# Kernel tuning notes

Hardware: AMD Instinct MI355X
Metric: run time of the kernel (lower is better)

Reference implementation:

```python
import jax, jax.numpy as jnp
import numpy as np

HEADS = 4
LN_EPS = 1e-5

def layernorm(x, w, b):
    m = x.mean(-1, keepdims=True)
    v = ((x - m) ** 2).mean(-1, keepdims=True)
    return (x - m) * jax.lax.rsqrt(v + LN_EPS) * w + b

def conv3d(x, w, b, pad, dil=1, groups=1):
    out = jax.lax.conv_general_dilated(
        x, w, (1, 1, 1), [(pad, pad)] * 3,
        rhs_dilation=(dil, dil, dil),
        dimension_numbers=('NCDHW', 'OIDHW', 'NCDHW'),
        feature_group_count=groups)
    return out + b[None, :, None, None, None]

def trilinear_gather(x_flat, pz, py, px, D, H, W):
    # x_flat: [B,C,S]; pz/py/px: [B,S] fractional sample coords, zero padding outside
    z0f, y0f, x0f = jnp.floor(pz), jnp.floor(py), jnp.floor(px)
    wz, wy, wx = pz - z0f, py - y0f, px - x0f
    z0, y0, x0 = z0f.astype(jnp.int32), y0f.astype(jnp.int32), x0f.astype(jnp.int32)
    acc = jnp.zeros_like(x_flat)
    for dz in (0, 1):
        for dy in (0, 1):
            for dx in (0, 1):
                iz, iy, ix = z0 + dz, y0 + dy, x0 + dx
                cw = (wz if dz else 1.0 - wz) * (wy if dy else 1.0 - wy) * (wx if dx else 1.0 - wx)
                valid = (iz >= 0) & (iz < D) & (iy >= 0) & (iy < H) & (ix >= 0) & (ix < W)
                idx = (jnp.clip(iz, 0, D - 1) * H + jnp.clip(iy, 0, H - 1)) * W + jnp.clip(ix, 0, W - 1)
                vals = jnp.take_along_axis(x_flat, idx[:, None, :], axis=2)
                acc = acc + vals * (cw * valid)[:, None, :]
    return acc

def deform_conv3d(x, off_w, off_b, w, b):
    # DeformConvPack: offsets from a regular 3x3x3 conv, then offset trilinear sampling + conv
    B, C, D, H, W = x.shape
    K = 27
    offsets = conv3d(x, off_w, off_b, 1).reshape(B, K, 3, D * H * W)
    gz, gy, gx = jnp.indices((D, H, W))
    bz = gz.reshape(-1).astype(x.dtype)[None]
    by = gy.reshape(-1).astype(x.dtype)[None]
    bx = gx.reshape(-1).astype(x.dtype)[None]
    x_flat = x.reshape(B, C, -1)
    O = w.shape[0]
    wk = w.reshape(O, C, K)
    out = jnp.zeros((B, O, D * H * W), x.dtype)
    for k in range(K):  # fixed 27 kernel taps
        kz, ky, kx = k // 9, (k // 3) % 3, k % 3
        pz = bz + (kz - 1) + offsets[:, k, 0]
        py = by + (ky - 1) + offsets[:, k, 1]
        px = bx + (kx - 1) + offsets[:, k, 2]
        samp = trilinear_gather(x_flat, pz, py, px, D, H, W)  # [B,C,S]
        out = out + jnp.einsum('bcs,oc->bos', samp, wk[:, :, k])
    out = out + b[None, :, None]
    return out.reshape(B, O, D, H, W)

def forward(x, temperature, qkv_w, norm_w, norm_b, proj1_w, proj1_b, conv0_w, conv0_b,
            convsp_w, convsp_b, off_w, off_b, dcn_w, dcn_b, conv1_w, conv1_b,
            proj2_w, proj2_b, norm2_w, norm2_b, out_w, out_b, H, W, D):
    B, N, C = x.shape
    hd = C // HEADS
    qkv = (x @ qkv_w.T).reshape(B, N, 3, HEADS, hd).transpose(2, 0, 3, 1, 4)  # [3,B,h,N,hd]
    q = qkv[0].transpose(0, 1, 3, 2)  # [B,h,hd,N]
    k = qkv[1].transpose(0, 1, 3, 2)
    v = qkv[2].transpose(0, 1, 3, 2)
    q = q / jnp.maximum(jnp.sqrt((q * q).sum(-1, keepdims=True)), 1e-12)
    k = k / jnp.maximum(jnp.sqrt((k * k).sum(-1, keepdims=True)), 1e-12)
    attn = jnp.einsum('bhcn,bhdn->bhcd', q, k) * temperature[None]
    attn = jax.nn.softmax(attn, axis=-1)
    x_ca = jnp.einsum('bhcd,bhdn->bhcn', attn, v).transpose(0, 3, 1, 2).reshape(B, N, C)
    x_ca = layernorm(x_ca, norm_w, norm_b)
    x5 = x_ca.transpose(0, 2, 1).reshape(B, C, H, W, D)
    shortcut = x5
    y = jnp.einsum('bcxyz,oc->boxyz', x5, proj1_w) + proj1_b[None, :, None, None, None]
    y = jax.nn.gelu(y, approximate=False)
    u = y
    a = conv3d(y, conv0_w, conv0_b, 2, 1, C)      # depthwise k=5 pad=2
    a = conv3d(a, convsp_w, convsp_b, 9, 3, C)    # depthwise k=7 pad=9 dil=3
    a = deform_conv3d(a, off_w, off_b, dcn_w, dcn_b)
    a = jnp.einsum('bcxyz,oc->boxyz', a, conv1_w) + conv1_b[None, :, None, None, None]
    y = u * a
    y = jnp.einsum('bcxyz,oc->boxyz', y, proj2_w) + proj2_b[None, :, None, None, None]
    y = y + shortcut
    x_sa = y.reshape(B, C, N).transpose(0, 2, 1)           # lka returns [B,N,C]
    x_sa = x_sa.reshape(B, C, N).transpose(0, 2, 1)        # faithful torch reshape-after-permute
    x_sa = layernorm(x_sa, norm2_w, norm2_b)
    return x_sa @ out_w.T + out_b

def setup_inputs():
    key = jax.random.key(0)
    ks = jax.random.split(key, 12)
    B, C, H, W, D = 2, 64, 32, 32, 32
    N = H * W * D
    s = 0.02
    return dict(
        x=jax.random.normal(ks[0], (B, N, C), jnp.float32),
        temperature=jnp.ones((HEADS, 1, 1), jnp.float32),
        qkv_w=jax.random.normal(ks[1], (3 * C, C), jnp.float32) * s,
        norm_w=jnp.ones((C,), jnp.float32), norm_b=jnp.zeros((C,), jnp.float32),
        proj1_w=jax.random.normal(ks[2], (C, C), jnp.float32) * s,
        proj1_b=jnp.zeros((C,), jnp.float32),
        conv0_w=jax.random.normal(ks[3], (C, 1, 5, 5, 5), jnp.float32) * s,
        conv0_b=jnp.zeros((C,), jnp.float32),
        convsp_w=jax.random.normal(ks[4], (C, 1, 7, 7, 7), jnp.float32) * s,
        convsp_b=jnp.zeros((C,), jnp.float32),
        off_w=jax.random.normal(ks[5], (81, C, 3, 3, 3), jnp.float32) * 0.01,
        off_b=jnp.zeros((81,), jnp.float32),
        dcn_w=jax.random.normal(ks[6], (C, C, 3, 3, 3), jnp.float32) * s,
        dcn_b=jnp.zeros((C,), jnp.float32),
        conv1_w=jax.random.normal(ks[7], (C, C), jnp.float32) * s,
        conv1_b=jnp.zeros((C,), jnp.float32),
        proj2_w=jax.random.normal(ks[8], (C, C), jnp.float32) * s,
        proj2_b=jnp.zeros((C,), jnp.float32),
        norm2_w=jnp.ones((C,), jnp.float32), norm2_b=jnp.zeros((C,), jnp.float32),
        out_w=jax.random.normal(ks[9], (C, C), jnp.float32) * s,
        out_b=jnp.zeros((C,), jnp.float32),
        B_in=B, C_in=C, H=H, W=W, D=D,
    )

def reference(x, temperature, qkv_w, norm_w, norm_b, proj1_w, proj1_b, conv0_w, conv0_b,
              convsp_w, convsp_b, off_w, off_b, dcn_w, dcn_b, conv1_w, conv1_b,
              proj2_w, proj2_b, norm2_w, norm2_b, out_w, out_b, B_in, C_in, H, W, D):
    return forward(x, temperature, qkv_w, norm_w, norm_b, proj1_w, proj1_b, conv0_w, conv0_b,
                   convsp_w, convsp_b, off_w, off_b, dcn_w, dcn_b, conv1_w, conv1_b,
                   proj2_w, proj2_b, norm2_w, norm2_b, out_w, out_b, H, W, D)
```

## Files before the change

kernel.cpp:

```cpp
#include <hip/hip_runtime.h>
#include <hip/hip_bf16.h>

#define S 32768
#define BUFN (2*64*32768)

typedef __bf16 v8bf __attribute__((ext_vector_type(8)));
typedef float v4f __attribute__((ext_vector_type(4)));
typedef int v4i __attribute__((ext_vector_type(4)));

__device__ __forceinline__ ushort f2b(float f) {
  union { float f; unsigned u; } v; v.f = f;
  unsigned r = (v.u + 0x7fffu + ((v.u >> 16) & 1u)) >> 16;
  return (ushort)r;
}
__device__ __forceinline__ float b2f(ushort h) {
  union { unsigned u; float f; } v; v.u = ((unsigned)h) << 16;
  return v.f;
}
__device__ __forceinline__ float u2f(unsigned u) {
  union { unsigned u; float f; } v; v.u = u;
  return v.f;
}

__global__ void k_wt(const float* __restrict__ offw, const float* __restrict__ dcnw,
                     ushort* __restrict__ wt_off16, ushort* __restrict__ wt_dcn16) {
  int i = blockIdx.x*256 + threadIdx.x;
  if (i < 27*96*64) {
    int c = i & 63, o = (i >> 6) % 96, t = i / 6144;
    wt_off16[i] = (o < 81) ? f2b(offw[o*1728 + c*27 + t]) : (ushort)0;
  }
  if (i < 27*64*64) {
    int c = i & 63, o = (i >> 6) & 63, k = i >> 12;
    wt_dcn16[i] = f2b(dcnw[(o*64 + c)*27 + k]);
  }
}

__global__ __launch_bounds__(256) void k_qkv(const float* __restrict__ x,
    const float* __restrict__ qkv_w, float* __restrict__ q,
    float* __restrict__ k, float* __restrict__ v) {
  __shared__ float wsm[96*64];
  int half = blockIdx.x >> 8;
  int gid  = ((blockIdx.x & 255) << 8) + threadIdx.x;
  int rbase = half * 96;
  for (int i = threadIdx.x; i < 96*64; i += 256) wsm[i] = qkv_w[rbase*64 + i];
  __syncthreads();
  int b = gid >> 15, n = gid & (S-1);
  const float* xr = x + (size_t)gid * 64;
  float xv[64];
#pragma unroll
  for (int i = 0; i < 16; i++) {
    float4 t = ((const float4*)xr)[i];
    xv[4*i]=t.x; xv[4*i+1]=t.y; xv[4*i+2]=t.z; xv[4*i+3]=t.w;
  }
  for (int r = 0; r < 96; r++) {
    const float4* wr4 = (const float4*)&wsm[r*64];
    float acc = 0.f;
#pragma unroll
    for (int c4 = 0; c4 < 16; c4++) {
      float4 wv4 = wr4[c4];
      acc += xv[4*c4]*wv4.x + xv[4*c4+1]*wv4.y + xv[4*c4+2]*wv4.z + xv[4*c4+3]*wv4.w;
    }
    int row = rbase + r;
    float* dst = (row < 64) ? q : (row < 128 ? k : v);
    int ch = row & 63;
    dst[((size_t)(b*64 + ch))*S + n] = acc;
  }
}

__global__ __launch_bounds__(256) void k_rownorm(const float* __restrict__ q,
    const float* __restrict__ k, float* __restrict__ inv) {
  int row = blockIdx.x;
  const float* p = (row < 128) ? (q + (size_t)row*S) : (k + (size_t)(row-128)*S);
  const float4* p4 = (const float4*)p;
  float ss = 0.f;
  for (int i = threadIdx.x; i < S/4; i += 256) {
    float4 t = p4[i];
    ss += t.x*t.x + t.y*t.y + t.z*t.z + t.w*t.w;
  }
  __shared__ float red[256];
  red[threadIdx.x] = ss; __syncthreads();
  for (int st = 128; st > 0; st >>= 1) {
    if (threadIdx.x < st) red[threadIdx.x] += red[threadIdx.x+st];
    __syncthreads();
  }
  if (threadIdx.x == 0) inv[row] = 1.0f / fmaxf(sqrtf(red[0]), 1e-12f);
}

__global__ __launch_bounds__(256) void k_gram(const float* __restrict__ q,
    const float* __restrict__ k, float* __restrict__ gram) {
  __shared__ float qt[16][65], kt[16][65];
  int bi = blockIdx.x;
  int b = bi >> 7, h = (bi >> 5) & 3, chunk = bi & 31;
  int c = threadIdx.x >> 4, d = threadIdx.x & 15;
  const float* qb = q + ((size_t)(b*64 + h*16))*S;
  const float* kb = k + ((size_t)(b*64 + h*16))*S;
  int lr = threadIdx.x >> 4, lc = (threadIdx.x & 15) * 4;
  float acc = 0.f;
  for (int n0 = chunk*1024; n0 < chunk*1024 + 1024; n0 += 64) {
    float4 tq = *(const float4*)(qb + (size_t)lr*S + n0 + lc);
    float4 tk = *(const float4*)(kb + (size_t)lr*S + n0 + lc);
    __syncthreads();
    qt[lr][lc]=tq.x; qt[lr][lc+1]=tq.y; qt[lr][lc+2]=tq.z; qt[lr][lc+3]=tq.w;
    kt[lr][lc]=tk.x; kt[lr][lc+1]=tk.y; kt[lr][lc+2]=tk.z; kt[lr][lc+3]=tk.w;
    __syncthreads();
#pragma unroll
    for (int nn = 0; nn < 64; nn++) acc += qt[c][nn]*kt[d][nn];
  }
  atomicAdd(&gram[((b*4+h)*16+c)*16 + d], acc);
}

__global__ __launch_bounds__(256) void k_xca_ln(const float* __restrict__ v,
    const float* __restrict__ gram, const float* __restrict__ inv,
    const float* __restrict__ temp,
    const float* __restrict__ nw, const float* __restrict__ nb,
    float* __restrict__ x5) {
  __shared__ float at[1024];
  __shared__ float wsh[64], bsh[64];
  int gid = blockIdx.x*256 + threadIdx.x;
  int b = gid >> 15, n = gid & (S-1);
  int tid = threadIdx.x;
  if (tid < 64) {
    int h = tid >> 4, c = tid & 15;
    float iq = inv[b*64 + h*16 + c];
    float tp = temp[h];
    float l[16], m = -1e30f;
#pragma unroll
    for (int d = 0; d < 16; d++) {
      float vv = gram[((b*4+h)*16+c)*16 + d] * iq * inv[128 + b*64 + h*16 + d] * tp;
      l[d] = vv; m = fmaxf(m, vv);
    }
    float s = 0.f;
#pragma unroll
    for (int d = 0; d < 16; d++) { l[d] = expf(l[d]-m); s += l[d]; }
    float is = 1.0f / s;
#pragma unroll
    for (int d = 0; d < 16; d++) at[(h*16+c)*16 + d] = l[d]*is;
  } else if (tid < 128) {
    wsh[tid-64] = nw[tid-64]; bsh[tid-64] = nb[tid-64];
  }
  __syncthreads();
  const float* vb = v + (size_t)b*64*S + n;
  float vv[64];
#pragma unroll
  for (int ch = 0; ch < 64; ch++) vv[ch] = vb[(size_t)ch*S];
  float xc[64];
#pragma unroll
  for (int h = 0; h < 4; h++)
#pragma unroll
    for (int cc = 0; cc < 16; cc++) {
      float a = 0.f;
#pragma unroll
      for (int d = 0; d < 16; d++) a += at[(h*16+cc)*16 + d] * vv[h*16+d];
      xc[h*16+cc] = a;
    }
  float mean = 0.f;
#pragma unroll
  for (int ch = 0; ch < 64; ch++) mean += xc[ch];
  mean *= (1.0f/64.0f);
  float var = 0.f;
#pragma unroll
  for (int ch = 0; ch < 64; ch++) { float d = xc[ch]-mean; var += d*d; }
  var *= (1.0f/64.0f);
  float rs = rsqrtf(var + 1e-5f);
  float* xb = x5 + (size_t)b*64*S + n;
#pragma unroll
  for (int ch = 0; ch < 64; ch++)
    xb[(size_t)ch*S] = (xc[ch]-mean)*rs*wsh[ch] + bsh[ch];
}

__global__ __launch_bounds__(256) void k_proj1(const float* __restrict__ x5,
    const float* __restrict__ w, const float* __restrict__ bias, float* __restrict__ u) {
  __shared__ float wsm[32*64];
  __shared__ float bsm[32];
  int half = blockIdx.x >> 8;
  int gid = ((blockIdx.x & 255) << 8) + threadIdx.x;
  int o0 = half*32;
  for (int i = threadIdx.x; i < 32*64; i += 256) wsm[i] = w[o0*64 + i];
  if (threadIdx.x < 32) bsm[threadIdx.x] = bias[o0 + threadIdx.x];
  __syncthreads();
  int b = gid >> 15, n = gid & (S-1);
  const float* xb = x5 + (size_t)b*64*S + n;
  float xv[64];
#pragma unroll
  for (int ch = 0; ch < 64; ch++) xv[ch] = xb[(size_t)ch*S];
  float* ub = u + (size_t)b*64*S + n;
  for (int oo = 0; oo < 32; oo++) {
    const float4* wr4 = (const float4*)&wsm[oo*64];
    float acc = bsm[oo];
#pragma unroll
    for (int c4 = 0; c4 < 16; c4++) {
      float4 wv4 = wr4[c4];
      acc += xv[4*c4]*wv4.x + xv[4*c4+1]*wv4.y + xv[4*c4+2]*wv4.z + xv[4*c4+3]*wv4.w;
    }
    float g = 0.5f*acc*(1.0f + erff(acc*0.70710678118654752f));
    ub[(size_t)(o0+oo)*S] = g;
  }
}

__global__ __launch_bounds__(256) void k_conv0(const float* __restrict__ in,
    const float* __restrict__ w, const float* __restrict__ bias, ushort* __restrict__ out) {
  __shared__ ushort tile[5*32*40];
  __shared__ float wsh[128];
  int bi = blockIdx.x;
  int z = bi & 31, c = (bi >> 5) & 63, b = bi >> 11;
  const float* ib = in + ((size_t)(b*64+c) << 15);
  for (int i = threadIdx.x; i < 800; i += 256)
    ((int4*)tile)[i] = make_int4(0,0,0,0);
  if (threadIdx.x < 125) wsh[threadIdx.x] = w[c*125 + threadIdx.x];
  __syncthreads();
  for (int i = threadIdx.x; i < 5*1024; i += 256) {
    int dz = i >> 10, r = i & 1023;
    int zg = z + dz - 2;
    if (zg >= 0 && zg < 32)
      tile[(dz*32 + (r >> 5))*40 + (r & 31) + 2] = f2b(ib[zg*1024 + r]);
  }
  __syncthreads();
  int y = threadIdx.x >> 3, x0 = (threadIdx.x & 7) << 2;
  float bv = bias[c];
  float acc[4] = {bv, bv, bv, bv};
  for (int dz = 0; dz < 5; dz++) {
#pragma unroll
    for (int dy = 0; dy < 5; dy++) {
      int yy = y + dy - 2;
      if (yy < 0 || yy >= 32) continue;
      const float* wp = &wsh[(dz*5+dy)*5];
      float wreg[5];
#pragma unroll
      for (int dx = 0; dx < 5; dx++) wreg[dx] = wp[dx];
      const ushort* rp = &tile[(dz*32+yy)*40 + x0];
      int2 rl = *(const int2*)rp;
      int2 rh = *(const int2*)(rp + 4);
      float row[8];
      row[0]=u2f(((unsigned)rl.x)<<16); row[1]=u2f(rl.x & 0xffff0000u);
      row[2]=u2f(((unsigned)rl.y)<<16); row[3]=u2f(rl.y & 0xffff0000u);
      row[4]=u2f(((unsigned)rh.x)<<16); row[5]=u2f(rh.x & 0xffff0000u);
      row[6]=u2f(((unsigned)rh.y)<<16); row[7]=u2f(rh.y & 0xffff0000u);
#pragma unroll
      for (int dx = 0; dx < 5; dx++)
#pragma unroll
        for (int j = 0; j < 4; j++)
          acc[j] += wreg[dx] * row[dx+j];
    }
  }
  ushort* ob = out + ((size_t)(b*64+c) << 15) + z*1024 + y*32 + x0;
  unsigned p0 = (unsigned)f2b(acc[0]) | ((unsigned)f2b(acc[1]) << 16);
  unsigned p1 = (unsigned)f2b(acc[2]) | ((unsigned)f2b(acc[3]) << 16);
  *(int2*)ob = make_int2((int)p0, (int)p1);
}

__global__ __launch_bounds__(256) void k_convsp(const ushort* __restrict__ in,
    const float* __restrict__ w, const float* __restrict__ bias, ushort* __restrict__ out) {
  __shared__ ushort tile[7*32*56];
  __shared__ float wsh[344];
  int bi = blockIdx.x;
  int z = bi & 31, c = (bi >> 5) & 63, b = bi >> 11;
  const ushort* ib = in + ((size_t)(b*64+c) << 15);
  for (int i = threadIdx.x; i < 1568; i += 256)
    ((int4*)tile)[i] = make_int4(0,0,0,0);
  for (int i = threadIdx.x; i < 343; i += 256) wsh[i] = w[c*343 + i];
  __syncthreads();
  for (int i = threadIdx.x; i < 7*1024; i += 256) {
    int t = i >> 10, r = i & 1023;
    int zg = z + 3*t - 9;
    if (zg >= 0 && zg < 32)
      tile[(t*32 + (r >> 5))*56 + (r & 31) + 9] = ib[zg*1024 + r];
  }
  __syncthreads();
  int y = threadIdx.x >> 3, x0 = (threadIdx.x & 7) << 2;
  float bv = bias[c];
  float acc[4] = {bv, bv, bv, bv};
  for (int t = 0; t < 7; t++) {
#pragma unroll
    for (int dy = 0; dy < 7; dy++) {
      int yy = y + 3*dy - 9;
      if (yy < 0 || yy >= 32) continue;
      const float* wp = &wsh[(t*7+dy)*7];
      float wreg[7];
#pragma unroll
      for (int dx = 0; dx < 7; dx++) wreg[dx] = wp[dx];
      const ushort* rp = &tile[(t*32+yy)*56 + x0];
      float row[24];
#pragma unroll
      for (int qq = 0; qq < 6; qq++) {
        int2 rv = *(const int2*)(rp + 4*qq);
        row[4*qq+0]=u2f(((unsigned)rv.x)<<16); row[4*qq+1]=u2f(rv.x & 0xffff0000u);
        row[4*qq+2]=u2f(((unsigned)rv.y)<<16); row[4*qq+3]=u2f(rv.y & 0xffff0000u);
      }
#pragma unroll
      for (int dx = 0; dx < 7; dx++)
#pragma unroll
        for (int j = 0; j < 4; j++)
          acc[j] += wreg[dx] * row[3*dx+j];
    }
  }
  ushort* ob = out + ((size_t)(b*64+c) << 15) + z*1024 + y*32 + x0;
  unsigned p0 = (unsigned)f2b(acc[0]) | ((unsigned)f2b(acc[1]) << 16);
  unsigned p1 = (unsigned)f2b(acc[2]) | ((unsigned)f2b(acc[3]) << 16);
  *(int2*)ob = make_int2((int)p0, (int)p1);
}

__global__ __launch_bounds__(256) void k_tr(const ushort* __restrict__ a2,
                                            ushort* __restrict__ a2t) {
  __shared__ ushort tile[64*66];
  int bi = blockIdx.x;
  int b = bi >> 9, chunk = bi & 511;
  int s0 = chunk << 6;
  const ushort* ib = a2 + ((size_t)b << 21) + s0;
#pragma unroll
  for (int i = 0; i < 16; i++) {
    int j = threadIdx.x + (i << 8);
    int c = j >> 6, sl = j & 63;
    tile[c*66 + sl] = ib[((size_t)c << 15) + sl];
  }
  __syncthreads();
  ushort* ob = a2t + ((size_t)b << 21) + ((size_t)s0 << 6);
#pragma unroll
  for (int i = 0; i < 16; i++) {
    int j = threadIdx.x + (i << 8);
    int sl = j >> 6, c = j & 63;
    ob[sl*64 + c] = tile[c*66 + sl];
  }
}

__global__ __launch_bounds__(256) void k_offconv(const ushort* __restrict__ a2t,
    const ushort* __restrict__ wt16, float* __restrict__ off) {
  int bi = blockIdx.x;
  int b = bi >> 9, tile = bi & 511;
  int s0 = tile << 6;
  int tid = threadIdx.x;
  int lane = tid & 63, wv = tid >> 6;
  int si = lane & 15, rq = lane >> 4, q8 = rq << 3;
  int sw = s0 + (wv << 4);
  int s_c = sw + si;
  int zc = s_c >> 10, yc = (s_c >> 5) & 31, xc = s_c & 31;
  const ushort* a2b = a2t + ((size_t)b << 21);
  v4f acc[6];
#pragma unroll
  for (int i = 0; i < 6; i++) acc[i] = (v4f){0.f,0.f,0.f,0.f};
  const v4i z4 = {0,0,0,0};
  for (int t = 0; t < 27; t++) {
    int kz = t/9, ky = (t/3)%3, kx = t%3;
    int zz = zc + kz - 1, yy = yc + ky - 1, xx = xc + kx - 1;
    bool ok = (zz>=0 && zz<32 && yy>=0 && yy<32 && xx>=0 && xx<32);
    v8bf b0 = __builtin_bit_cast(v8bf, z4);
    v8bf b1 = __builtin_bit_cast(v8bf, z4);
    if (ok) {
      const ushort* p = a2b + ((size_t)((zz<<10)+(yy<<5)+xx) << 6) + q8;
      b0 = *(const v8bf*)p;
      b1 = *(const v8bf*)(p + 32);
    }
    const ushort* wk = wt16 + t*6144;
#pragma unroll
    for (int ot = 0; ot < 6; ot++) {
      const ushort* ap = wk + (((ot<<4) + si) << 6) + q8;
      v8bf a0 = *(const v8bf*)ap;
      v8bf a1 = *(const v8bf*)(ap + 32);
      acc[ot] = __builtin_amdgcn_mfma_f32_16x16x32_bf16(a0, b0, acc[ot], 0,0,0);
      acc[ot] = __builtin_amdgcn_mfma_f32_16x16x32_bf16(a1, b1, acc[ot], 0,0,0);
    }
  }
#pragma unroll
  for (int ot = 0; ot < 6; ot++)
#pragma unroll
    for (int r = 0; r < 4; r++) {
      int o = ot*16 + rq*4 + r;
      if (o < 81)
        off[(((size_t)(b*81 + o)) << 15) + sw + si] = acc[ot][r];
    }
}

__global__ __launch_bounds__(256) void k_dcn(const ushort* __restrict__ a2t,
    const float* __restrict__ off, const float* __restrict__ off_b,
    const ushort* __restrict__ wt16, float* __restrict__ out) {
  __shared__ float ofs[81*66];
  __shared__ ushort scr[4][16*72];
  int bi = blockIdx.x;
  int b = bi >> 9, tile = bi & 511;
  int s0 = tile << 6;
  int tid = threadIdx.x;
  const float* offbase = off + (((size_t)(b*81)) << 15) + s0;
  for (int i = tid; i < 5184; i += 256) {
    int r = i >> 6, sl = i & 63;
    ofs[r*66 + sl] = offbase[((size_t)r << 15) + sl] + off_b[r];
  }
  __syncthreads();
  int lane = tid & 63, wv = tid >> 6;
  int sr = lane >> 3, cs = lane & 7;
  int si = lane & 15, rq = lane >> 4;
  int sw = s0 + (wv << 4);
  const ushort* a2b = a2t + ((size_t)b << 21);
  ushort* myscr = &scr[wv][0];
  int sA = sw + sr, sB = sw + 8 + sr;
  int zA = sA >> 10, yA = (sA >> 5) & 31, xA = sA & 31;
  int zB = sB >> 10, yB = (sB >> 5) & 31, xB = sB & 31;
  int slcA = (wv << 4) + sr, slcB = slcA + 8;
  v4f acc[4];
#pragma unroll
  for (int t = 0; t < 4; t++) acc[t] = (v4f){0.f,0.f,0.f,0.f};
  for (int k = 0; k < 27; k++) {
    int kz = k/9, ky = (k/3)%3, kx = k%3;
    int idxA[8], idxB[8];
    float wA[8], wB[8];
    {
      float pz = (float)(zA + kz - 1) + ofs[(3*k+0)*66 + slcA];
      float py = (float)(yA + ky - 1) + ofs[(3*k+1)*66 + slcA];
      float px = (float)(xA + kx - 1) + ofs[(3*k+2)*66 + slcA];
      float fz = floorf(pz), fy = floorf(py), fx = floorf(px);
      float wz = pz-fz, wy = py-fy, wx = px-fx;
      int z0 = (int)fz, y0 = (int)fy, x0 = (int)fx;
      int zi[2], yi[2], xi[2]; float zw[2], yw[2], xw[2];
#pragma unroll
      for (int d = 0; d < 2; d++) {
        int iz = z0 + d; zi[d] = min(max(iz,0),31) << 10;
        zw[d] = (iz >= 0 && iz < 32) ? (d ? wz : 1.f-wz) : 0.f;
        int iy = y0 + d; yi[d] = min(max(iy,0),31) << 5;
        yw[d] = (iy >= 0 && iy < 32) ? (d ? wy : 1.f-wy) : 0.f;
        int ix = x0 + d; xi[d] = min(max(ix,0),31);
        xw[d] = (ix >= 0 && ix < 32) ? (d ? wx : 1.f-wx) : 0.f;
      }
#pragma unroll
      for (int r = 0; r < 8; r++) {
        int dz = r >> 2, dy = (r >> 1) & 1, dx = r & 1;
        idxA[r] = zi[dz] + yi[dy] + xi[dx];
        wA[r] = zw[dz] * yw[dy] * xw[dx];
      }
    }
    {
      float pz = (float)(zB + kz - 1) + ofs[(3*k+0)*66 + slcB];
      float py = (float)(yB + ky - 1) + ofs[(3*k+1)*66 + slcB];
      float px = (float)(xB + kx - 1) + ofs[(3*k+2)*66 + slcB];
      float fz = floorf(pz), fy = floorf(py), fx = floorf(px);
      float wz = pz-fz, wy = py-fy, wx = px-fx;
      int z0 = (int)fz, y0 = (int)fy, x0 = (int)fx;
      int zi[2], yi[2], xi[2]; float zw[2], yw[2], xw[2];
#pragma unroll
      for (int d = 0; d < 2; d++) {
        int iz = z0 + d; zi[d] = min(max(iz,0),31) << 10;
        zw[d] = (iz >= 0 && iz < 32) ? (d ? wz : 1.f-wz) : 0.f;
        int iy = y0 + d; yi[d] = min(max(iy,0),31) << 5;
        yw[d] = (iy >= 0 && iy < 32) ? (d ? wy : 1.f-wy) : 0.f;
        int ix = x0 + d; xi[d] = min(max(ix,0),31);
        xw[d] = (ix >= 0 && ix < 32) ? (d ? wx : 1.f-wx) : 0.f;
      }
#pragma unroll
      for (int r = 0; r < 8; r++) {
        int dz = r >> 2, dy = (r >> 1) & 1, dx = r & 1;
        idxB[r] = zi[dz] + yi[dy] + xi[dx];
        wB[r] = zw[dz] * yw[dy] * xw[dx];
      }
    }
    v4i gA[8], gB[8];
#pragma unroll
    for (int r = 0; r < 8; r++)
      gA[r] = *(const v4i*)(a2b + ((size_t)idxA[r] << 6) + (cs << 3));
#pragma unroll
    for (int r = 0; r < 8; r++)
      gB[r] = *(const v4i*)(a2b + ((size_t)idxB[r] << 6) + (cs << 3));
    float faA[8], faB[8];
#pragma unroll
    for (int j = 0; j < 8; j++) { faA[j] = 0.f; faB[j] = 0.f; }
#pragma unroll
    for (int r = 0; r < 8; r++) {
      float wa = wA[r], wb = wB[r];
#pragma unroll
      for (int m = 0; m < 4; m++) {
        unsigned da = (unsigned)gA[r][m];
        faA[2*m]   += wa * u2f(da << 16);
        faA[2*m+1] += wa * u2f(da & 0xffff0000u);
        unsigned db = (unsigned)gB[r][m];
        faB[2*m]   += wb * u2f(db << 16);
        faB[2*m+1] += wb * u2f(db & 0xffff0000u);
      }
    }
    v4i dA, dB;
#pragma unroll
    for (int m = 0; m < 4; m++) {
      unsigned l0 = (__float_as_uint(faA[2*m])   + 0x8000u) >> 16;
      unsigned h0 = (__float_as_uint(faA[2*m+1]) + 0x8000u) & 0xffff0000u;
      dA[m] = (int)(l0 | h0);
      unsigned l1 = (__float_as_uint(faB[2*m])   + 0x8000u) >> 16;
      unsigned h1 = (__float_as_uint(faB[2*m+1]) + 0x8000u) & 0xffff0000u;
      dB[m] = (int)(l1 | h1);
    }
    *(v4i*)&myscr[sr*72 + (cs << 3)]       = dA;
    *(v4i*)&myscr[(8+sr)*72 + (cs << 3)]   = dB;
    v8bf bf0 = *(const v8bf*)&myscr[si*72 + (rq << 3)];
    v8bf bf1 = *(const v8bf*)&myscr[si*72 + 32 + (rq << 3)];
    const ushort* wk = wt16 + (k << 12);
#pragma unroll
    for (int ot = 0; ot < 4; ot++) {
      const ushort* ap = wk + (((ot<<4) + si) << 6) + (rq << 3);
      v8bf a0 = *(const v8bf*)ap;
      v8bf a1 = *(const v8bf*)(ap + 32);
      acc[ot] = __builtin_amdgcn_mfma_f32_16x16x32_bf16(a0, bf0, acc[ot], 0,0,0);
      acc[ot] = __builtin_amdgcn_mfma_f32_16x16x32_bf16(a1, bf1, acc[ot], 0,0,0);
    }
  }
#pragma unroll
  for (int ot = 0; ot < 4; ot++)
#pragma unroll
    for (int r = 0; r < 4; r++) {
      int o = (ot << 4) + rq*4 + r;
      out[(((size_t)(b*64 + o)) << 15) + sw + si] = acc[ot][r];
    }
}

__global__ __launch_bounds__(256) void k_fuse2(const float* __restrict__ dcn0,
    const float* __restrict__ dcn_b, const float* __restrict__ c1w,
    const float* __restrict__ c1b, const float* __restrict__ u,
    const float* __restrict__ p2w, const float* __restrict__ p2b,
    const float* __restrict__ x5, float* __restrict__ y2) {
  __shared__ float w1[4096], w2[4096];
  __shared__ float b1[64], b2[64], db[64];
  int gid = blockIdx.x*256 + threadIdx.x;
  for (int i = threadIdx.x; i < 4096; i += 256) { w1[i] = c1w[i]; w2[i] = p2w[i]; }
  if (threadIdx.x < 64) {
    b1[threadIdx.x]=c1b[threadIdx.x]; b2[threadIdx.x]=p2b[threadIdx.x];
    db[threadIdx.x]=dcn_b[threadIdx.x];
  }
  __syncthreads();
  int b = gid >> 15, n = gid & (S-1);
  const float* dbp0 = dcn0 + (size_t)b*64*S + n;
  float dv[64];
#pragma unroll
  for (int c = 0; c < 64; c++)
    dv[c] = dbp0[(size_t)c*S] + db[c];
  const float* ub = u + (size_t)b*64*S + n;
  float m[64];
  for (int o = 0; o < 64; o++) {
    const float4* w4 = (const float4*)&w1[o*64];
    float a = b1[o];
#pragma unroll
    for (int c4 = 0; c4 < 16; c4++) {
      float4 wv4 = w4[c4];
      a += dv[4*c4]*wv4.x + dv[4*c4+1]*wv4.y + dv[4*c4+2]*wv4.z + dv[4*c4+3]*wv4.w;
    }
    m[o] = ub[(size_t)o*S] * a;
  }
  const float* sb = x5 + (size_t)b*64*S + n;
  float* yb = y2 + (size_t)b*64*S + n;
  for (int o = 0; o < 64; o++) {
    const float4* w4 = (const float4*)&w2[o*64];
    float a = b2[o];
#pragma unroll
    for (int c4 = 0; c4 < 16; c4++) {
      float4 wv4 = w4[c4];
      a += m[4*c4]*wv4.x + m[4*c4+1]*wv4.y + m[4*c4+2]*wv4.z + m[4*c4+3]*wv4.w;
    }
    yb[(size_t)o*S] = a + sb[(size_t)o*S];
  }
}

__global__ __launch_bounds__(256) void k_final(const float* __restrict__ y2,
    const float* __restrict__ n2w, const float* __restrict__ n2b,
    const float* __restrict__ ow, const float* __restrict__ ob, float* __restrict__ out) {
  __shared__ float wsh[4096];
  __shared__ float nw[64], nb[64], obs[64];
  int bi = blockIdx.x;
  int b = bi >> 7; int mg = (bi >> 4) & 7; int r0 = (bi & 15)*4;
  for (int i = threadIdx.x; i < 4096; i += 256) wsh[i] = ow[i];
  if (threadIdx.x < 64) {
    nw[threadIdx.x]=n2w[threadIdx.x]; nb[threadIdx.x]=n2b[threadIdx.x];
    obs[threadIdx.x]=ob[threadIdx.x];
  }
  __syncthreads();
  int mi = threadIdx.x & 63, rg = threadIdx.x >> 6;
  int r = r0 + rg;
  int m = mg*64 + mi;
  int n = m*64 + r;
  const float* yb = y2 + ((size_t)(b*64+r))*S + m;
  float v[64];
#pragma unroll
  for (int c = 0; c < 64; c++) v[c] = yb[(size_t)c*512];
  float mean = 0.f;
#pragma unroll
  for (int c = 0; c < 64; c++) mean += v[c];
  mean *= (1.0f/64.0f);
  float var = 0.f;
#pragma unroll
  for (int c = 0; c < 64; c++) { float d = v[c]-mean; var += d*d; }
  var *= (1.0f/64.0f);
  float rs = rsqrtf(var + 1e-5f);
#pragma unroll
  for (int c = 0; c < 64; c++) v[c] = (v[c]-mean)*rs*nw[c] + nb[c];
  float* orow = out + ((size_t)b*S + n)*64;
  for (int o4 = 0; o4 < 16; o4++) {
    const float4* w0 = (const float4*)&wsh[(o4*4+0)*64];
    const float4* w1 = (const float4*)&wsh[(o4*4+1)*64];
    const float4* w2 = (const float4*)&wsh[(o4*4+2)*64];
    const float4* w3 = (const float4*)&wsh[(o4*4+3)*64];
    float t0=obs[o4*4+0], t1=obs[o4*4+1], t2=obs[o4*4+2], t3=obs[o4*4+3];
#pragma unroll
    for (int c4 = 0; c4 < 16; c4++) {
      float4 a0 = w0[c4], a1 = w1[c4], a2 = w2[c4], a3 = w3[c4];
      float v0 = v[4*c4], v1 = v[4*c4+1], v2 = v[4*c4+2], v3 = v[4*c4+3];
      t0 += a0.x*v0 + a0.y*v1 + a0.z*v2 + a0.w*v3;
      t1 += a1.x*v0 + a1.y*v1 + a1.z*v2 + a1.w*v3;
      t2 += a2.x*v0 + a2.y*v1 + a2.z*v2 + a2.w*v3;
      t3 += a3.x*v0 + a3.y*v1 + a3.z*v2 + a3.w*v3;
    }
    float4 a; a.x=t0; a.y=t1; a.z=t2; a.w=t3;
    ((float4*)orow)[o4] = a;
  }
}

extern "C" void kernel_launch(void* const* d_in, const int* in_sizes, int n_in,
                              void* d_out, int out_size, void* d_ws, size_t ws_size,
                              hipStream_t stream) {
  const float* x      = (const float*)d_in[0];
  const float* temp   = (const float*)d_in[1];
  const float* qkv_w  = (const float*)d_in[2];
  const float* norm_w = (const float*)d_in[3];
  const float* norm_b = (const float*)d_in[4];
  const float* p1w    = (const float*)d_in[5];
  const float* p1b    = (const float*)d_in[6];
  const float* c0w    = (const float*)d_in[7];
  const float* c0b    = (const float*)d_in[8];
  const float* cspw   = (const float*)d_in[9];
  const float* cspb   = (const float*)d_in[10];
  const float* offw   = (const float*)d_in[11];
  const float* offb   = (const float*)d_in[12];
  const float* dcnw   = (const float*)d_in[13];
  const float* dcnb   = (const float*)d_in[14];
  const float* c1w    = (const float*)d_in[15];
  const float* c1b    = (const float*)d_in[16];
  const float* p2w    = (const float*)d_in[17];
  const float* p2b    = (const float*)d_in[18];
  const float* n2w    = (const float*)d_in[19];
  const float* n2b    = (const float*)d_in[20];
  const float* outw   = (const float*)d_in[21];
  const float* outb   = (const float*)d_in[22];
  float* out = (float*)d_out;

  float* Wa  = (float*)d_ws;
  float* Wb  = Wa + BUFN;
  float* Wc  = Wb + BUFN;
  float* OFF = Wc + BUFN;
  float* SM  = OFF + (size_t)2*81*S;
  float* SM_inv  = SM;
  float* SM_gram = SM + 256;
  ushort* WT_OFF16 = (ushort*)(SM + 4352);
  ushort* WT_DCN16 = WT_OFF16 + 165888;
  float* vbuf = out;
  ushort* A1_16 = (ushort*)d_out;
  ushort* A2_16 = (ushort*)Wc;
  ushort* a2t = (ushort*)d_out;

  hipMemsetAsync(SM, 0, 4352*sizeof(float), stream);
  k_wt     <<<648, 256, 0, stream>>>(offw, dcnw, WT_OFF16, WT_DCN16);

  k_qkv    <<<512, 256, 0, stream>>>(x, qkv_w, Wa, Wb, vbuf);
  k_rownorm<<<256, 256, 0, stream>>>(Wa, Wb, SM_inv);
  k_gram   <<<256, 256, 0, stream>>>(Wa, Wb, SM_gram);
  k_xca_ln <<<256, 256, 0, stream>>>(vbuf, SM_gram, SM_inv, temp, norm_w, norm_b, Wa);
  k_proj1  <<<512, 256, 0, stream>>>(Wa, p1w, p1b, Wb);
  k_conv0  <<<4096,256, 0, stream>>>(Wb, c0w, c0b, A1_16);
  k_convsp <<<4096,256, 0, stream>>>(A1_16, cspw, cspb, A2_16);
  k_tr     <<<1024,256, 0, stream>>>(A2_16, a2t);
  k_offconv<<<1024,256, 0, stream>>>(a2t, WT_OFF16, OFF);
  k_dcn    <<<1024,256, 0, stream>>>(a2t, OFF, offb, WT_DCN16, Wc);
  k_fuse2  <<<256, 256, 0, stream>>>(Wc, dcnb, c1w, c1b, Wb, p2w, p2b, Wa, OFF);
  k_final  <<<256, 256, 0, stream>>>(OFF, n2w, n2b, outw, outb, out);
}
```

Baseline: 833.7 us.

## Read uniform weights directly from global memory instead of staging in LDS

Removes the per-block shared-memory staging of weights and biases, plus the barrier after it, from the qkv, proj1, conv0, convsp, fuse2 and final kernels. These kernels now read the weights straight from global memory, relying on uniform scalar or cached loads. The per-batch attention softmax moves out of every xca_ln block into one tiny separate kernel that writes the attention matrix once. This cuts redundant LDS fills and the softmax work each block repeated, at the cost of one extra launch. It also risks slower weight reads if the compiler does not turn them into scalar loads.

```diff
diff --git a/kernel.cpp b/kernel.cpp
--- a/kernel.cpp
+++ b/kernel.cpp
@@ -38,12 +38,9 @@
 __global__ __launch_bounds__(256) void k_qkv(const float* __restrict__ x,
     const float* __restrict__ qkv_w, float* __restrict__ q,
     float* __restrict__ k, float* __restrict__ v) {
-  __shared__ float wsm[96*64];
   int half = blockIdx.x >> 8;
   int gid  = ((blockIdx.x & 255) << 8) + threadIdx.x;
   int rbase = half * 96;
-  for (int i = threadIdx.x; i < 96*64; i += 256) wsm[i] = qkv_w[rbase*64 + i];
-  __syncthreads();
   int b = gid >> 15, n = gid & (S-1);
   const float* xr = x + (size_t)gid * 64;
   float xv[64];
@@ -53,7 +50,7 @@
     xv[4*i]=t.x; xv[4*i+1]=t.y; xv[4*i+2]=t.z; xv[4*i+3]=t.w;
   }
   for (int r = 0; r < 96; r++) {
-    const float4* wr4 = (const float4*)&wsm[r*64];
+    const float4* wr4 = (const float4*)(qkv_w + (size_t)(rbase + r)*64);
     float acc = 0.f;
 #pragma unroll
     for (int c4 = 0; c4 < 16; c4++) {
@@ -109,36 +106,33 @@
   atomicAdd(&gram[((b*4+h)*16+c)*16 + d], acc);
 }
 
+__global__ void k_attnsm(const float* __restrict__ gram, const float* __restrict__ inv,
+    const float* __restrict__ temp, float* __restrict__ attn) {
+  int t = threadIdx.x; if (t >= 128) return;
+  int b = t >> 6, h = (t >> 4) & 3, c = t & 15;
+  float iq = inv[b*64 + h*16 + c];
+  float tp = temp[h];
+  float l[16], m = -1e30f;
+#pragma unroll
+  for (int d = 0; d < 16; d++) {
+    float vv = gram[((b*4+h)*16+c)*16 + d] * iq * inv[128 + b*64 + h*16 + d] * tp;
+    l[d] = vv; m = fmaxf(m, vv);
+  }
+  float s = 0.f;
+#pragma unroll
+  for (int d = 0; d < 16; d++) { l[d] = expf(l[d]-m); s += l[d]; }
+  float is = 1.0f / s;
+#pragma unroll
+  for (int d = 0; d < 16; d++) attn[((b*4+h)*16+c)*16 + d] = l[d]*is;
+}
+
 __global__ __launch_bounds__(256) void k_xca_ln(const float* __restrict__ v,
-    const float* __restrict__ gram, const float* __restrict__ inv,
-    const float* __restrict__ temp,
+    const float* __restrict__ attn,
     const float* __restrict__ nw, const float* __restrict__ nb,
     float* __restrict__ x5) {
-  __shared__ float at[1024];
-  __shared__ float wsh[64], bsh[64];
   int gid = blockIdx.x*256 + threadIdx.x;
   int b = gid >> 15, n = gid & (S-1);
-  int tid = threadIdx.x;
-  if (tid < 64) {
-    int h = tid >> 4, c = tid & 15;
-    float iq = inv[b*64 + h*16 + c];
-    float tp = temp[h];
-    float l[16], m = -1e30f;
-#pragma unroll
-    for (int d = 0; d < 16; d++) {
-      float vv = gram[((b*4+h)*16+c)*16 + d] * iq * inv[128 + b*64 + h*16 + d] * tp;
-      l[d] = vv; m = fmaxf(m, vv);
-    }
-    float s = 0.f;
-#pragma unroll
-    for (int d = 0; d < 16; d++) { l[d] = expf(l[d]-m); s += l[d]; }
-    float is = 1.0f / s;
-#pragma unroll
-    for (int d = 0; d < 16; d++) at[(h*16+c)*16 + d] = l[d]*is;
-  } else if (tid < 128) {
-    wsh[tid-64] = nw[tid-64]; bsh[tid-64] = nb[tid-64];
-  }
-  __syncthreads();
+  const float* at = attn + b*1024;
   const float* vb = v + (size_t)b*64*S + n;
   float vv[64];
 #pragma unroll
@@ -165,19 +159,14 @@
   float* xb = x5 + (size_t)b*64*S + n;
 #pragma unroll
   for (int ch = 0; ch < 64; ch++)
-    xb[(size_t)ch*S] = (xc[ch]-mean)*rs*wsh[ch] + bsh[ch];
+    xb[(size_t)ch*S] = (xc[ch]-mean)*rs*nw[ch] + nb[ch];
 }
 
 __global__ __launch_bounds__(256) void k_proj1(const float* __restrict__ x5,
     const float* __restrict__ w, const float* __restrict__ bias, float* __restrict__ u) {
-  __shared__ float wsm[32*64];
-  __shared__ float bsm[32];
   int half = blockIdx.x >> 8;
   int gid = ((blockIdx.x & 255) << 8) + threadIdx.x;
   int o0 = half*32;
-  for (int i = threadIdx.x; i < 32*64; i += 256) wsm[i] = w[o0*64 + i];
-  if (threadIdx.x < 32) bsm[threadIdx.x] = bias[o0 + threadIdx.x];
-  __syncthreads();
   int b = gid >> 15, n = gid & (S-1);
   const float* xb = x5 + (size_t)b*64*S + n;
   float xv[64];
@@ -185,8 +174,8 @@
   for (int ch = 0; ch < 64; ch++) xv[ch] = xb[(size_t)ch*S];
   float* ub = u + (size_t)b*64*S + n;
   for (int oo = 0; oo < 32; oo++) {
-    const float4* wr4 = (const float4*)&wsm[oo*64];
-    float acc = bsm[oo];
+    const float4* wr4 = (const float4*)(w + (size_t)(o0+oo)*64);
+    float acc = bias[o0+oo];
 #pragma unroll
     for (int c4 = 0; c4 < 16; c4++) {
       float4 wv4 = wr4[c4];
@@ -200,13 +189,12 @@
 __global__ __launch_bounds__(256) void k_conv0(const float* __restrict__ in,
     const float* __restrict__ w, const float* __restrict__ bias, ushort* __restrict__ out) {
   __shared__ ushort tile[5*32*40];
-  __shared__ float wsh[128];
   int bi = blockIdx.x;
   int z = bi & 31, c = (bi >> 5) & 63, b = bi >> 11;
   const float* ib = in + ((size_t)(b*64+c) << 15);
+  const float* wc = w + c*125;
   for (int i = threadIdx.x; i < 800; i += 256)
     ((int4*)tile)[i] = make_int4(0,0,0,0);
-  if (threadIdx.x < 125) wsh[threadIdx.x] = w[c*125 + threadIdx.x];
   __syncthreads();
   for (int i = threadIdx.x; i < 5*1024; i += 256) {
     int dz = i >> 10, r = i & 1023;
@@ -223,7 +211,7 @@
     for (int dy = 0; dy < 5; dy++) {
       int yy = y + dy - 2;
       if (yy < 0 || yy >= 32) continue;
-      const float* wp = &wsh[(dz*5+dy)*5];
+      const float* wp = wc + (dz*5+dy)*5;
       float wreg[5];
 #pragma unroll
       for (int dx = 0; dx < 5; dx++) wreg[dx] = wp[dx];
@@ -251,13 +239,12 @@
 __global__ __launch_bounds__(256) void k_convsp(const ushort* __restrict__ in,
     const float* __restrict__ w, const float* __restrict__ bias, ushort* __restrict__ out) {
   __shared__ ushort tile[7*32*56];
-  __shared__ float wsh[344];
   int bi = blockIdx.x;
   int z = bi & 31, c = (bi >> 5) & 63, b = bi >> 11;
   const ushort* ib = in + ((size_t)(b*64+c) << 15);
+  const float* wc = w + c*343;
   for (int i = threadIdx.x; i < 1568; i += 256)
     ((int4*)tile)[i] = make_int4(0,0,0,0);
-  for (int i = threadIdx.x; i < 343; i += 256) wsh[i] = w[c*343 + i];
   __syncthreads();
   for (int i = threadIdx.x; i < 7*1024; i += 256) {
     int t = i >> 10, r = i & 1023;
@@ -274,7 +261,7 @@
     for (int dy = 0; dy < 7; dy++) {
       int yy = y + 3*dy - 9;
       if (yy < 0 || yy >= 32) continue;
-      const float* wp = &wsh[(t*7+dy)*7];
+      const float* wp = wc + (t*7+dy)*7;
       float wreg[7];
 #pragma unroll
       for (int dx = 0; dx < 7; dx++) wreg[dx] = wp[dx];
@@ -510,26 +497,18 @@
     const float* __restrict__ c1b, const float* __restrict__ u,
     const float* __restrict__ p2w, const float* __restrict__ p2b,
     const float* __restrict__ x5, float* __restrict__ y2) {
-  __shared__ float w1[4096], w2[4096];
-  __shared__ float b1[64], b2[64], db[64];
   int gid = blockIdx.x*256 + threadIdx.x;
-  for (int i = threadIdx.x; i < 4096; i += 256) { w1[i] = c1w[i]; w2[i] = p2w[i]; }
-  if (threadIdx.x < 64) {
-    b1[threadIdx.x]=c1b[threadIdx.x]; b2[threadIdx.x]=p2b[threadIdx.x];
-    db[threadIdx.x]=dcn_b[threadIdx.x];
-  }
-  __syncthreads();
   int b = gid >> 15, n = gid & (S-1);
   const float* dbp0 = dcn0 + (size_t)b*64*S + n;
   float dv[64];
 #pragma unroll
   for (int c = 0; c < 64; c++)
-    dv[c] = dbp0[(size_t)c*S] + db[c];
+    dv[c] = dbp0[(size_t)c*S] + dcn_b[c];
   const float* ub = u + (size_t)b*64*S + n;
   float m[64];
   for (int o = 0; o < 64; o++) {
-    const float4* w4 = (const float4*)&w1[o*64];
-    float a = b1[o];
+    const float4* w4 = (const float4*)(c1w + (size_t)o*64);
+    float a = c1b[o];
 #pragma unroll
     for (int c4 = 0; c4 < 16; c4++) {
       float4 wv4 = w4[c4];
@@ -540,8 +519,8 @@
   const float* sb = x5 + (size_t)b*64*S + n;
   float* yb = y2 + (size_t)b*64*S + n;
   for (int o = 0; o < 64; o++) {
-    const float4* w4 = (const float4*)&w2[o*64];
-    float a = b2[o];
+    const float4* w4 = (const float4*)(p2w + (size_t)o*64);
+    float a = p2b[o];
 #pragma unroll
     for (int c4 = 0; c4 < 16; c4++) {
       float4 wv4 = w4[c4];
@@ -554,16 +533,8 @@
 __global__ __launch_bounds__(256) void k_final(const float* __restrict__ y2,
     const float* __restrict__ n2w, const float* __restrict__ n2b,
     const float* __restrict__ ow, const float* __restrict__ ob, float* __restrict__ out) {
-  __shared__ float wsh[4096];
-  __shared__ float nw[64], nb[64], obs[64];
   int bi = blockIdx.x;
   int b = bi >> 7; int mg = (bi >> 4) & 7; int r0 = (bi & 15)*4;
-  for (int i = threadIdx.x; i < 4096; i += 256) wsh[i] = ow[i];
-  if (threadIdx.x < 64) {
-    nw[threadIdx.x]=n2w[threadIdx.x]; nb[threadIdx.x]=n2b[threadIdx.x];
-    obs[threadIdx.x]=ob[threadIdx.x];
-  }
-  __syncthreads();
   int mi = threadIdx.x & 63, rg = threadIdx.x >> 6;
   int r = r0 + rg;
   int m = mg*64 + mi;
@@ -582,14 +553,14 @@
   var *= (1.0f/64.0f);
   float rs = rsqrtf(var + 1e-5f);
 #pragma unroll
-  for (int c = 0; c < 64; c++) v[c] = (v[c]-mean)*rs*nw[c] + nb[c];
+  for (int c = 0; c < 64; c++) v[c] = (v[c]-mean)*rs*n2w[c] + n2b[c];
   float* orow = out + ((size_t)b*S + n)*64;
   for (int o4 = 0; o4 < 16; o4++) {
-    const float4* w0 = (const float4*)&wsh[(o4*4+0)*64];
-    const float4* w1 = (const float4*)&wsh[(o4*4+1)*64];
-    const float4* w2 = (const float4*)&wsh[(o4*4+2)*64];
-    const float4* w3 = (const float4*)&wsh[(o4*4+3)*64];
-    float t0=obs[o4*4+0], t1=obs[o4*4+1], t2=obs[o4*4+2], t3=obs[o4*4+3];
+    const float4* w0 = (const float4*)(ow + (size_t)(o4*4+0)*64);
+    const float4* w1 = (const float4*)(ow + (size_t)(o4*4+1)*64);
+    const float4* w2 = (const float4*)(ow + (size_t)(o4*4+2)*64);
+    const float4* w3 = (const float4*)(ow + (size_t)(o4*4+3)*64);
+    float t0=ob[o4*4+0], t1=ob[o4*4+1], t2=ob[o4*4+2], t3=ob[o4*4+3];
 #pragma unroll
     for (int c4 = 0; c4 < 16; c4++) {
       float4 a0 = w0[c4], a1 = w1[c4], a2 = w2[c4], a3 = w3[c4];
@@ -639,6 +610,7 @@
   float* SM  = OFF + (size_t)2*81*S;
   float* SM_inv  = SM;
   float* SM_gram = SM + 256;
+  float* SM_attn = SM + 2304;
   ushort* WT_OFF16 = (ushort*)(SM + 4352);
   ushort* WT_DCN16 = WT_OFF16 + 165888;
   float* vbuf = out;
@@ -652,7 +624,8 @@
   k_qkv    <<<512, 256, 0, stream>>>(x, qkv_w, Wa, Wb, vbuf);
   k_rownorm<<<256, 256, 0, stream>>>(Wa, Wb, SM_inv);
   k_gram   <<<256, 256, 0, stream>>>(Wa, Wb, SM_gram);
-  k_xca_ln <<<256, 256, 0, stream>>>(vbuf, SM_gram, SM_inv, temp, norm_w, norm_b, Wa);
+  k_attnsm <<<1,   128, 0, stream>>>(SM_gram, SM_inv, temp, SM_attn);
+  k_xca_ln <<<256, 256, 0, stream>>>(vbuf, SM_attn, norm_w, norm_b, Wa);
   k_proj1  <<<512, 256, 0, stream>>>(Wa, p1w, p1b, Wb);
   k_conv0  <<<4096,256, 0, stream>>>(Wb, c0w, c0b, A1_16);
   k_convsp <<<4096,256, 0, stream>>>(A1_16, cspw, cspb, A2_16);
```

New measurement: 925.7 us. +11.0%, slower.

## Split deformable conv taps across two block groups to double parallelism

Applied to the files above, without the earlier changes.

The deformable conv kernel now launches twice as many blocks. Each group handles half of the 27 kernel taps (0-13 or 14-26) and stages only its own offset rows in shared memory, which also roughly halves LDS use per block. The first group writes fp32 partial sums and the second writes bf16 partial sums into the spare half of the output buffer. The fuse kernel adds the two partials together. This is meant to raise occupancy and the number of blocks in flight for a latency-bound gather kernel, at the cost of an extra partial-sum read and write and bf16 rounding of half the accumulation.

```diff
diff --git a/kernel.cpp b/kernel.cpp
--- a/kernel.cpp
+++ b/kernel.cpp
@@ -371,17 +371,21 @@
 
 __global__ __launch_bounds__(256) void k_dcn(const ushort* __restrict__ a2t,
     const float* __restrict__ off, const float* __restrict__ off_b,
-    const ushort* __restrict__ wt16, float* __restrict__ out) {
-  __shared__ float ofs[81*66];
+    const ushort* __restrict__ wt16, float* __restrict__ out0,
+    ushort* __restrict__ out1) {
+  __shared__ float ofs[42*66];
   __shared__ ushort scr[4][16*72];
   int bi = blockIdx.x;
-  int b = bi >> 9, tile = bi & 511;
+  int kg = bi >> 10;
+  int b = (bi >> 9) & 1, tile = bi & 511;
   int s0 = tile << 6;
   int tid = threadIdx.x;
+  int kbeg = kg ? 14 : 0, kend = kg ? 27 : 14;
+  int r0 = 3*kbeg, nrows = 3*(kend - kbeg);
   const float* offbase = off + (((size_t)(b*81)) << 15) + s0;
-  for (int i = tid; i < 5184; i += 256) {
+  for (int i = tid; i < nrows*64; i += 256) {
     int r = i >> 6, sl = i & 63;
-    ofs[r*66 + sl] = offbase[((size_t)r << 15) + sl] + off_b[r];
+    ofs[r*66 + sl] = offbase[((size_t)(r0 + r) << 15) + sl] + off_b[r0 + r];
   }
   __syncthreads();
   int lane = tid & 63, wv = tid >> 6;
@@ -397,14 +401,15 @@
   v4f acc[4];
 #pragma unroll
   for (int t = 0; t < 4; t++) acc[t] = (v4f){0.f,0.f,0.f,0.f};
-  for (int k = 0; k < 27; k++) {
+  for (int k = kbeg; k < kend; k++) {
     int kz = k/9, ky = (k/3)%3, kx = k%3;
+    int kr = 3*k - r0;
     int idxA[8], idxB[8];
     float wA[8], wB[8];
     {
-      float pz = (float)(zA + kz - 1) + ofs[(3*k+0)*66 + slcA];
-      float py = (float)(yA + ky - 1) + ofs[(3*k+1)*66 + slcA];
-      float px = (float)(xA + kx - 1) + ofs[(3*k+2)*66 + slcA];
+      float pz = (float)(zA + kz - 1) + ofs[(kr+0)*66 + slcA];
+      float py = (float)(yA + ky - 1) + ofs[(kr+1)*66 + slcA];
+      float px = (float)(xA + kx - 1) + ofs[(kr+2)*66 + slcA];
       float fz = floorf(pz), fy = floorf(py), fx = floorf(px);
       float wz = pz-fz, wy = py-fy, wx = px-fx;
       int z0 = (int)fz, y0 = (int)fy, x0 = (int)fx;
@@ -426,9 +431,9 @@
       }
     }
     {
-      float pz = (float)(zB + kz - 1) + ofs[(3*k+0)*66 + slcB];
-      float py = (float)(yB + ky - 1) + ofs[(3*k+1)*66 + slcB];
-      float px = (float)(xB + kx - 1) + ofs[(3*k+2)*66 + slcB];
+      float pz = (float)(zB + kz - 1) + ofs[(kr+0)*66 + slcB];
+      float py = (float)(yB + ky - 1) + ofs[(kr+1)*66 + slcB];
+      float px = (float)(xB + kx - 1) + ofs[(kr+2)*66 + slcB];
       float fz = floorf(pz), fy = floorf(py), fx = floorf(px);
       float wz = pz-fz, wy = py-fy, wx = px-fx;
       int z0 = (int)fz, y0 = (int)fy, x0 = (int)fx;
@@ -496,16 +501,27 @@
       acc[ot] = __builtin_amdgcn_mfma_f32_16x16x32_bf16(a1, bf1, acc[ot], 0,0,0);
     }
   }
-#pragma unroll
-  for (int ot = 0; ot < 4; ot++)
-#pragma unroll
-    for (int r = 0; r < 4; r++) {
-      int o = (ot << 4) + rq*4 + r;
-      out[(((size_t)(b*64 + o)) << 15) + sw + si] = acc[ot][r];
-    }
+  if (kg == 0) {
+#pragma unroll
+    for (int ot = 0; ot < 4; ot++)
+#pragma unroll
+      for (int r = 0; r < 4; r++) {
+        int o = (ot << 4) + rq*4 + r;
+        out0[(((size_t)(b*64 + o)) << 15) + sw + si] = acc[ot][r];
+      }
+  } else {
+#pragma unroll
+    for (int ot = 0; ot < 4; ot++)
+#pragma unroll
+      for (int r = 0; r < 4; r++) {
+        int o = (ot << 4) + rq*4 + r;
+        out1[(((size_t)(b*64 + o)) << 15) + sw + si] = f2b(acc[ot][r]);
+      }
+  }
 }
 
 __global__ __launch_bounds__(256) void k_fuse2(const float* __restrict__ dcn0,
+    const ushort* __restrict__ dcn1,
     const float* __restrict__ dcn_b, const float* __restrict__ c1w,
     const float* __restrict__ c1b, const float* __restrict__ u,
     const float* __restrict__ p2w, const float* __restrict__ p2b,
@@ -521,10 +537,11 @@
   __syncthreads();
   int b = gid >> 15, n = gid & (S-1);
   const float* dbp0 = dcn0 + (size_t)b*64*S + n;
+  const ushort* dbp1 = dcn1 + (size_t)b*64*S + n;
   float dv[64];
 #pragma unroll
   for (int c = 0; c < 64; c++)
-    dv[c] = dbp0[(size_t)c*S] + db[c];
+    dv[c] = dbp0[(size_t)c*S] + b2f(dbp1[(size_t)c*S]) + db[c];
   const float* ub = u + (size_t)b*64*S + n;
   float m[64];
   for (int o = 0; o < 64; o++) {
@@ -645,6 +662,7 @@
   ushort* A1_16 = (ushort*)d_out;
   ushort* A2_16 = (ushort*)Wc;
   ushort* a2t = (ushort*)d_out;
+  ushort* dcn1 = a2t + ((size_t)1 << 22);
 
   hipMemsetAsync(SM, 0, 4352*sizeof(float), stream);
   k_wt     <<<648, 256, 0, stream>>>(offw, dcnw, WT_OFF16, WT_DCN16);
@@ -658,7 +676,7 @@
   k_convsp <<<4096,256, 0, stream>>>(A1_16, cspw, cspb, A2_16);
   k_tr     <<<1024,256, 0, stream>>>(A2_16, a2t);
   k_offconv<<<1024,256, 0, stream>>>(a2t, WT_OFF16, OFF);
-  k_dcn    <<<1024,256, 0, stream>>>(a2t, OFF, offb, WT_DCN16, Wc);
-  k_fuse2  <<<256, 256, 0, stream>>>(Wc, dcnb, c1w, c1b, Wb, p2w, p2b, Wa, OFF);
+  k_dcn    <<<2048,256, 0, stream>>>(a2t, OFF, offb, WT_DCN16, Wc, dcn1);
+  k_fuse2  <<<256, 256, 0, stream>>>(Wc, dcn1, dcnb, c1w, c1b, Wb, p2w, p2b, Wa, OFF);
   k_final  <<<256, 256, 0, stream>>>(OFF, n2w, n2b, outw, outb, out);
 }
```

Result: no change. 840.5 us (+0.8%).
